# Optimization experiments

Measured on AMD Instinct MI355X. Metric: run time of the kernel, lower is better.

The kernel has to match this reference:

```python
import jax, jax.numpy as jnp
import numpy as np
import math

C = 512
GROUPS = 32
EPS = 1e-06


def group_norm(x, w, b):
    # x: [B, C, H, W]; 32 groups over channels
    B, Cc, H, W = x.shape
    xg = x.reshape(B, GROUPS, Cc // GROUPS, H, W)
    mu = jnp.mean(xg, axis=(2, 3, 4), keepdims=True)
    var = jnp.var(xg, axis=(2, 3, 4), keepdims=True)
    xn = ((xg - mu) * jax.lax.rsqrt(var + EPS)).reshape(B, Cc, H, W)
    return xn * w[None, :, None, None] + b[None, :, None, None]


def setup_inputs() -> dict:
    key = jax.random.key(0)
    ks = jax.random.split(key, 7)
    B, H, W = 2, 64, 64
    x = jax.random.normal(ks[0], (B, C, H, W), dtype=jnp.float32)
    gn_w = jnp.ones((C,), dtype=jnp.float32)
    gn_b = jnp.zeros((C,), dtype=jnp.float32)
    s = 1.0 / math.sqrt(C)
    qkv_w = jax.random.normal(ks[1], (3 * C, C), dtype=jnp.float32) * s
    qkv_b = jnp.zeros((3 * C,), dtype=jnp.float32)
    proj_w = jax.random.normal(ks[2], (C, C), dtype=jnp.float32) * s
    proj_b = jnp.zeros((C,), dtype=jnp.float32)
    return {"x": x, "gn_w": gn_w, "gn_b": gn_b, "qkv_w": qkv_w,
            "qkv_b": qkv_b, "proj_w": proj_w, "proj_b": proj_b}


def reference(x, gn_w, gn_b, qkv_w, qkv_b, proj_w, proj_b):
    residue = x
    B, Cc, H, W = x.shape
    N = H * W
    constant = 1.0 / math.sqrt(Cc)
    xn = group_norm(x, gn_w, gn_b)
    # 1x1 conv == channel matmul
    qkv = jnp.einsum('bchw,oc->bohw', xn, qkv_w) + qkv_b[None, :, None, None]
    q, k, v = jnp.split(qkv, 3, axis=1)
    q = q.reshape(B, Cc, N)
    k = k.reshape(B, Cc, N)
    v = v.reshape(B, Cc, N)
    # attn[b,i,j] = sum_c k[b,c,i] * q[b,c,j]   (k^T @ q, per original code)
    attn = jnp.einsum('bci,bcj->bij', k, q) * constant
    soft = jax.nn.softmax(attn, axis=2)  # softmax over q-index j, as in torch dim=2
    # output[b,c,i] = sum_j v[b,c,j] * soft[b,j,i]   (v @ soft)
    out = jnp.einsum('bcj,bji->bci', v, soft).reshape(B, Cc, H, W)
    proj = jnp.einsum('bchw,oc->bohw', out, proj_w) + proj_b[None, :, None, None]
    return residue + proj
```

## Files before the change

### kernel.cpp

```cpp
#include <hip/hip_runtime.h>
#include <hip/hip_bf16.h>
#include <math.h>

typedef unsigned short ushort_t;
typedef __attribute__((ext_vector_type(8))) unsigned short ushort8;
typedef __attribute__((ext_vector_type(8))) __bf16 bf16x8;
typedef __attribute__((ext_vector_type(4))) float f32x4;

__device__ inline ushort_t f2b(float f) {
  __hip_bfloat16 h = __float2bfloat16(f);
  return __builtin_bit_cast(ushort_t, h);
}
__device__ inline float b2f(ushort_t u) {
  __hip_bfloat16 h = __builtin_bit_cast(__hip_bfloat16, u);
  return __bfloat162float(h);
}

__device__ inline void gload16(const ushort_t* g, ushort_t* l) {
  __builtin_amdgcn_global_load_lds(
      (const __attribute__((address_space(1))) unsigned int*)g,
      (__attribute__((address_space(3))) unsigned int*)l, 16, 0, 0);
}

__device__ inline void xcd_swz(int& bx, int& by, int& bz) {
  const int nx = gridDim.x, ny = gridDim.y;
  const int nwg = nx * ny * gridDim.z;
  const int orig = blockIdx.x + nx * (blockIdx.y + ny * blockIdx.z);
  const int q = nwg >> 3, r = nwg & 7, xcd = orig & 7, loc = orig >> 3;
  const int wg = (xcd < r ? xcd * (q + 1) : r * (q + 1) + (xcd - r) * q) + loc;
  bx = wg % nx;
  by = (wg / nx) % ny;
  bz = wg / (nx * ny);
}

__global__ __launch_bounds__(256) void prep_stats(
    const float* __restrict__ qkv_w, const float* __restrict__ proj_w,
    const float* __restrict__ x, ushort_t* __restrict__ qkvw,
    ushort_t* __restrict__ projw, float* __restrict__ stats) {
  const int tid = threadIdx.x;
  if (blockIdx.x < 4096) {
    int idx = blockIdx.x * 256 + tid;
    const int NQ = 1536 * 512;
    if (idx < NQ) {
      qkvw[idx] = f2b(qkv_w[idx]);
    } else {
      int j = idx - NQ;
      if (j < 512 * 512) projw[j] = f2b(proj_w[j]);
    }
    return;
  }
  const int bg = blockIdx.x - 4096;
  const float4* xv = (const float4*)(x + (size_t)bg * 65536);
  float s = 0.f, ss = 0.f;
  for (int i = tid; i < 16384; i += 256) {
    float4 v = xv[i];
    s += v.x + v.y + v.z + v.w;
    ss += v.x * v.x + v.y * v.y + v.z * v.z + v.w * v.w;
  }
  __shared__ float red[8];
  for (int off = 32; off > 0; off >>= 1) {
    s += __shfl_down(s, off);
    ss += __shfl_down(ss, off);
  }
  if ((tid & 63) == 0) { red[tid >> 6] = s; red[4 + (tid >> 6)] = ss; }
  __syncthreads();
  if (tid == 0) {
    float st = red[0] + red[1] + red[2] + red[3];
    float sst = red[4] + red[5] + red[6] + red[7];
    float mean = st * (1.f / 65536.f);
    float var = sst * (1.f / 65536.f) - mean * mean;
    stats[bg * 2] = mean;
    stats[bg * 2 + 1] = rsqrtf(var + 1e-6f);
  }
}

__global__ __launch_bounds__(256) void gn_apply_t(
    const float* __restrict__ x, const float* __restrict__ w,
    const float* __restrict__ bgn, const float* __restrict__ stats,
    ushort_t* __restrict__ xnT) {
  __shared__ ushort_t tile[64][68];
  const int b = blockIdx.z;
  const int p0 = blockIdx.x * 64, c0 = blockIdx.y * 64;
  const int tid = threadIdx.x;
  const float* xb = x + ((size_t)b * 512 + c0) * 4096 + p0;
  const int tc = tid >> 4, tp = (tid & 15) * 4;
#pragma unroll
  for (int pass = 0; pass < 4; ++pass) {
    int c = pass * 16 + tc;
    int cg = c0 + c;
    float mean = stats[(b * 32 + (cg >> 4)) * 2];
    float inv = stats[(b * 32 + (cg >> 4)) * 2 + 1];
    float wc = w[cg] * inv;
    float bc = bgn[cg] - mean * wc;
    float4 v = *(const float4*)(xb + (size_t)c * 4096 + tp);
    tile[c][tp] = f2b(v.x * wc + bc);
    tile[c][tp + 1] = f2b(v.y * wc + bc);
    tile[c][tp + 2] = f2b(v.z * wc + bc);
    tile[c][tp + 3] = f2b(v.w * wc + bc);
  }
  __syncthreads();
  const int c8 = (tid & 7) * 8;
#pragma unroll
  for (int pass = 0; pass < 2; ++pass) {
    int p = pass * 32 + (tid >> 3);
    ushort8 u;
#pragma unroll
    for (int e = 0; e < 8; ++e) u[e] = tile[c8 + e][p];
    *(ushort8*)(xnT + ((size_t)b * 4096 + p0 + p) * 512 + c0 + c8) = u;
  }
}

__global__ __launch_bounds__(512, 2) void gemm8(
    const ushort_t* __restrict__ A, const ushort_t* __restrict__ B,
    ushort_t* __restrict__ Cg, float* __restrict__ smp, int N, int K, int lda,
    int ldb, size_t sA, size_t sB, size_t sC, float scale) {
  __shared__ __align__(16) ushort_t smem[66560];
  ushort_t* Asl = smem;
  ushort_t* Bsl = smem + 32768;
  float* s_sum = (float*)(smem + 65536);

  int bx, by, bz;
  xcd_swz(bx, by, bz);
  const ushort_t* Ab = A + bz * sA;
  const ushort_t* Bb = B + bz * sB;
  const int bm0 = by * 256, bn0 = bx * 256;
  const int tid = threadIdx.x;
  const int w = tid >> 6, lane = tid & 63;
  const int wr = w >> 2, wc = w & 3;
  const int fr = lane & 15, fq = lane >> 4;

  const int srow = tid >> 3, scb = tid & 7;
  const int ssw = scb ^ (srow & 7);
  const ushort_t* aS = Ab + (size_t)(bm0 + srow) * lda + ssw * 8;
  const ushort_t* bS = Bb + (size_t)(bn0 + srow) * ldb + ssw * 8;

  auto stage_a = [&](int s, int kk) {
#pragma unroll
    for (int g = 0; g < 4; ++g)
      gload16(aS + (size_t)(g * 64) * lda + kk,
              &Asl[s * 16384 + g * 4096 + w * 512]);
  };
  auto stage_b = [&](int s, int kk) {
#pragma unroll
    for (int g = 0; g < 4; ++g)
      gload16(bS + (size_t)(g * 64) * ldb + kk,
              &Bsl[s * 16384 + g * 4096 + w * 512]);
  };

  f32x4 acc[8][4] = {};
  bf16x8 a_r[4][2], b_r[4][2];

  auto read_a = [&](int s, int mh) {
#pragma unroll
    for (int mi = 0; mi < 4; ++mi) {
      int row = wr * 128 + mh * 64 + mi * 16 + fr;
#pragma unroll
      for (int ks = 0; ks < 2; ++ks) {
        int blk = ((ks * 4 + fq) ^ (row & 7)) * 8;
        a_r[mi][ks] = *(const bf16x8*)&Asl[s * 16384 + row * 64 + blk];
      }
    }
  };
  auto read_b = [&](int s, int nh) {
#pragma unroll
    for (int ni = 0; ni < 2; ++ni) {
      int row = wc * 64 + nh * 32 + ni * 16 + fr;
#pragma unroll
      for (int ks = 0; ks < 2; ++ks) {
        int blk = ((ks * 4 + fq) ^ (row & 7)) * 8;
        b_r[nh * 2 + ni][ks] = *(const bf16x8*)&Bsl[s * 16384 + row * 64 + blk];
      }
    }
  };
  auto phase_mfma = [&](int mh, int nh) {
    __builtin_amdgcn_s_setprio(1);
#pragma unroll
    for (int ks = 0; ks < 2; ++ks)
#pragma unroll
      for (int mi = 0; mi < 4; ++mi)
#pragma unroll
        for (int ni = 0; ni < 2; ++ni)
          acc[mh * 4 + mi][nh * 2 + ni] =
              __builtin_amdgcn_mfma_f32_16x16x32_bf16(
                  a_r[mi][ks], b_r[nh * 2 + ni][ks],
                  acc[mh * 4 + mi][nh * 2 + ni], 0, 0, 0);
    __builtin_amdgcn_s_setprio(0);
  };

  const int nt = K >> 6;
  stage_b(0, 0);
  stage_a(0, 0);
  if (nt > 1) {
    stage_b(1, 64);
    stage_a(1, 64);
    asm volatile("s_waitcnt vmcnt(8)" ::: "memory");
  } else {
    asm volatile("s_waitcnt vmcnt(0)" ::: "memory");
  }
  __builtin_amdgcn_s_barrier();

  for (int t = 0; t < nt; ++t) {
    const int s = t & 1;
    const int kk2 = (t + 2) << 6;
    const bool st2 = (t + 2) < nt;
    read_b(s, 0);
    read_b(s, 1);
    read_a(s, 0);
    phase_mfma(0, 0);
    phase_mfma(0, 1);
    read_a(s, 1);
    phase_mfma(1, 0);
    __builtin_amdgcn_s_barrier();
    if (st2) {
      stage_b(s, kk2);
      stage_a(s, kk2);
    }
    phase_mfma(1, 1);
    if (st2)
      asm volatile("s_waitcnt vmcnt(8)" ::: "memory");
    else if (t + 1 < nt)
      asm volatile("s_waitcnt vmcnt(0)" ::: "memory");
    __builtin_amdgcn_s_barrier();
  }
  __syncthreads();

  const size_t cbase = (size_t)bz * sC;
  float csum[4] = {0.f, 0.f, 0.f, 0.f};
  ushort_t* tp = smem;
#pragma unroll
  for (int step = 0; step < 2; ++step) {
    if (wr == step) {
#pragma unroll
      for (int mi = 0; mi < 8; ++mi)
#pragma unroll
        for (int ni = 0; ni < 4; ++ni)
#pragma unroll
          for (int r = 0; r < 4; ++r) {
            int lr = mi * 16 + fq * 4 + r;
            int col = wc * 64 + ni * 16 + fr;
            float e = __expf(fminf(acc[mi][ni][r] * scale, 76.f));
            csum[ni] += e;
            int cblk = col >> 3;
            tp[lr * 256 + (((cblk ^ (lr & 7)) << 3) | (col & 7))] = f2b(e);
          }
    }
    __syncthreads();
#pragma unroll
    for (int k = 0; k < 8; ++k) {
      int row = (tid >> 5) + 16 * k;
      int cblk = tid & 31;
      ushort8 u = *(const ushort8*)&tp[row * 256 + ((cblk ^ (row & 7)) << 3)];
      size_t off =
          cbase + (size_t)(bm0 + step * 128 + row) * N + bn0 + cblk * 8;
      __builtin_nontemporal_store(u, (ushort8*)(Cg + off));
    }
    __syncthreads();
  }
#pragma unroll
  for (int ni = 0; ni < 4; ++ni) {
    float s = csum[ni];
    s += __shfl_xor(s, 16);
    s += __shfl_xor(s, 32);
    if (lane < 16) s_sum[wr * 256 + wc * 64 + ni * 16 + lane] = s;
  }
  __syncthreads();
  if (tid < 256) {
    smp[((size_t)bz * 16 + by) * 4096 + bn0 + tid] =
        s_sum[tid] + s_sum[256 + tid];
  }
}

template <int EPI, int SPLIT>
__global__ __launch_bounds__(256, 2) void gemm_pl(
    const ushort_t* __restrict__ A, const ushort_t* __restrict__ B,
    void* __restrict__ Cg, const float* __restrict__ bias,
    const float* __restrict__ colsc, int N, int K, int lda, int ldb,
    size_t sA, size_t sB, size_t sC, size_t sSp) {
  __shared__ __align__(16) ushort_t Al[2][128 * 64];
  __shared__ __align__(16) ushort_t Bl[2][128 * 64];
  __shared__ float s_alpha[128];
  int bx, by, bzt;
  xcd_swz(bx, by, bzt);
  const int bz = bzt / SPLIT, sp = bzt % SPLIT;
  const ushort_t* Ab = A + bz * sA + (size_t)sp * K;
  const ushort_t* Bb = B + bz * sB + (size_t)sp * K;
  const int bm0 = by * 128, bn0 = bx * 128;
  const int tid = threadIdx.x;
  const int w = tid >> 6, lane = tid & 63;
  const int wm = (w >> 1) * 64, wn = (w & 1) * 64;
  const int fr = lane & 15, fq = lane >> 4;

  if constexpr (EPI == 3) {
    if (tid < 128) {
      float S = 0.f;
#pragma unroll
      for (int rc = 0; rc < 16; ++rc)
        S += colsc[((size_t)bz * 16 + rc) * 4096 + bn0 + tid];
      s_alpha[tid] = 1.f / S;
    }
    asm volatile("s_waitcnt lgkmcnt(0)" ::: "memory");
  }

  const int srow = tid >> 3, scb = tid & 7;
  const int ssw = scb ^ (srow & 7);
  const ushort_t* aS = Ab + (size_t)(bm0 + srow) * lda + ssw * 8;
  const ushort_t* bS = Bb + (size_t)(bn0 + srow) * ldb + ssw * 8;

  auto stage = [&](int s, int kk) {
#pragma unroll
    for (int g = 0; g < 4; ++g)
      gload16(aS + (size_t)(g * 32) * lda + kk, &Al[s][g * 2048 + w * 512]);
#pragma unroll
    for (int g = 0; g < 4; ++g)
      gload16(bS + (size_t)(g * 32) * ldb + kk, &Bl[s][g * 2048 + w * 512]);
  };

  f32x4 acc[4][4] = {};
  bf16x8 a_r[4][2], b_r[4][2];

  const int nt = K >> 6;
  stage(0, 0);
  if (nt > 1) {
    stage(1, 64);
    asm volatile("s_waitcnt vmcnt(8)" ::: "memory");
  } else {
    asm volatile("s_waitcnt vmcnt(0)" ::: "memory");
  }
  __builtin_amdgcn_s_barrier();

  for (int t = 0; t < nt; ++t) {
    const int s = t & 1;
#pragma unroll
    for (int mi = 0; mi < 4; ++mi) {
      int row = wm + mi * 16 + fr;
#pragma unroll
      for (int ks = 0; ks < 2; ++ks) {
        int blk = ((ks * 4 + fq) ^ (row & 7)) * 8;
        a_r[mi][ks] = *(const bf16x8*)&Al[s][row * 64 + blk];
      }
    }
#pragma unroll
    for (int ni = 0; ni < 4; ++ni) {
      int row = wn + ni * 16 + fr;
#pragma unroll
      for (int ks = 0; ks < 2; ++ks) {
        int blk = ((ks * 4 + fq) ^ (row & 7)) * 8;
        b_r[ni][ks] = *(const bf16x8*)&Bl[s][row * 64 + blk];
      }
    }
    __builtin_amdgcn_s_barrier();
    __builtin_amdgcn_s_setprio(1);
#pragma unroll
    for (int ks = 0; ks < 2; ++ks)
#pragma unroll
      for (int mi = 0; mi < 4; ++mi)
#pragma unroll
        for (int ni = 0; ni < 2; ++ni)
          acc[mi][ni] = __builtin_amdgcn_mfma_f32_16x16x32_bf16(
              a_r[mi][ks], b_r[ni][ks], acc[mi][ni], 0, 0, 0);
    __builtin_amdgcn_s_setprio(0);
    __builtin_amdgcn_s_barrier();
    if (t + 2 < nt) stage(s, (t + 2) << 6);
    __builtin_amdgcn_s_setprio(1);
#pragma unroll
    for (int ks = 0; ks < 2; ++ks)
#pragma unroll
      for (int mi = 0; mi < 4; ++mi)
#pragma unroll
        for (int ni = 2; ni < 4; ++ni)
          acc[mi][ni] = __builtin_amdgcn_mfma_f32_16x16x32_bf16(
              a_r[mi][ks], b_r[ni][ks], acc[mi][ni], 0, 0, 0);
    __builtin_amdgcn_s_setprio(0);
    if (t + 2 < nt)
      asm volatile("s_waitcnt vmcnt(8)" ::: "memory");
    else if (t + 1 < nt)
      asm volatile("s_waitcnt vmcnt(0)" ::: "memory");
    __builtin_amdgcn_s_barrier();
  }

  const int r0 = (lane >> 4) * 4;
  const size_t cbase = (size_t)sp * sSp + (size_t)bz * sC;
#pragma unroll
  for (int mi = 0; mi < 4; mi++) {
#pragma unroll
    for (int r = 0; r < 4; r++) {
      int gm = bm0 + wm + mi * 16 + r0 + r;
#pragma unroll
      for (int ni = 0; ni < 4; ni++) {
        int gn = bn0 + wn + ni * 16 + fr;
        float v = acc[mi][ni][r];
        size_t off = cbase + (size_t)gm * N + gn;
        if constexpr (EPI == 0) {
          ((ushort_t*)Cg)[off] = f2b(v + bias[gn]);
        } else if constexpr (EPI == 3) {
          ((ushort_t*)Cg)[off] = f2b(v * s_alpha[gn - bn0]);
        } else {
          __builtin_nontemporal_store(f2b(v), (ushort_t*)Cg + off);
        }
      }
    }
  }
}

__global__ __launch_bounds__(256) void finalize(
    const ushort_t* __restrict__ part, const float* __restrict__ x,
    const float* __restrict__ pb, float* __restrict__ out) {
  __shared__ float tile[64][68];
  const int b = blockIdx.z;
  const int p0 = blockIdx.x * 64, o0 = blockIdx.y * 64;
  const int tid = threadIdx.x;
  const int tp = tid >> 2, to = (tid & 3) * 16;
  const size_t base = ((size_t)b * 4096 + p0 + tp) * 512 + o0 + to;
  ushort8 u0 = *(const ushort8*)(part + base);
  ushort8 u1 = *(const ushort8*)(part + base + 8);
  ushort8 v0 = *(const ushort8*)(part + 4194304 + base);
  ushort8 v1 = *(const ushort8*)(part + 4194304 + base + 8);
#pragma unroll
  for (int e = 0; e < 8; ++e) {
    tile[tp][to + e] = b2f(u0[e]) + b2f(v0[e]);
    tile[tp][to + 8 + e] = b2f(u1[e]) + b2f(v1[e]);
  }
  __syncthreads();
  const int wo = tid >> 2, wp = (tid & 3) * 16;
  float bias = pb[o0 + wo];
  const float* xr = x + ((size_t)b * 512 + o0 + wo) * 4096 + p0 + wp;
  float* orow = out + ((size_t)b * 512 + o0 + wo) * 4096 + p0 + wp;
#pragma unroll
  for (int e = 0; e < 16; ++e)
    orow[e] = tile[wp + e][wo] + xr[e] + bias;
}

extern "C" void kernel_launch(void* const* d_in, const int* in_sizes, int n_in,
                              void* d_out, int out_size, void* d_ws,
                              size_t ws_size, hipStream_t stream) {
  const float* x = (const float*)d_in[0];
  const float* gn_w = (const float*)d_in[1];
  const float* gn_b = (const float*)d_in[2];
  const float* qkv_w = (const float*)d_in[3];
  const float* qkv_b = (const float*)d_in[4];
  const float* proj_w = (const float*)d_in[5];
  const float* proj_b = (const float*)d_in[6];
  float* out = (float*)d_out;

  char* ws = (char*)d_ws;
  ushort_t* xnT   = (ushort_t*)(ws);
  ushort_t* Wpp   = (ushort_t*)(ws);
  ushort_t* qkvw  = (ushort_t*)(ws + 8388608);
  ushort_t* projw = (ushort_t*)(ws + 9961472);
  float*    stats = (float*)(ws + 10485760);
  ushort_t* qkvT  = (ushort_t*)(ws + 10486272);
  ushort_t* part  = (ushort_t*)(ws + 10486272);
  ushort_t* P     = (ushort_t*)(ws + 35652096);
  float*    smp   = (float*)(ws + 102760960);

  const float scale = 0.04419417382415922f;
  const size_t sXN = 2097152, sQKV = (size_t)4096 * 1536, sP = 16777216;

  prep_stats<<<4160, 256, 0, stream>>>(qkv_w, proj_w, x, qkvw, projw, stats);
  gn_apply_t<<<dim3(64, 8, 2), 256, 0, stream>>>(x, gn_w, gn_b, stats, xnT);
  gemm_pl<0, 1><<<dim3(12, 64, 1), 256, 0, stream>>>(
      xnT, qkvw, qkvT, qkv_b, nullptr, 1536, 512, 512, 512, 0, 0, 0, 0);
  gemm8<<<dim3(16, 16, 2), 512, 0, stream>>>(
      qkvT, qkvT + 512, P, smp, 4096, 512, 1536, 1536, sQKV, sQKV, sP, scale);
  gemm_pl<3, 1><<<dim3(32, 4, 2), 256, 0, stream>>>(
      projw, qkvT + 1024, Wpp, nullptr, smp, 4096, 512, 512, 1536, 0, sQKV,
      sXN, 0);
  gemm_pl<5, 2><<<dim3(4, 32, 4), 256, 0, stream>>>(
      P, Wpp, part, nullptr, nullptr, 512, 2048, 4096, 4096, sP, sXN, sXN,
      4194304);
  finalize<<<dim3(64, 8, 2), 256, 0, stream>>>(part, x, proj_b, out);
}
```

Before: 172.3 us.

## Halve gemm K-tile to 32 to cut LDS and raise occupancy

Shrinks the GEMM K-step from 64 to 32, halving shared memory per block (about 66 KB down to 33 KB) and raising launch bounds to allow 4 blocks per CU. Staging, swizzle and fragment loads are rewritten for 32-wide rows, and the MFMA loop is restructured so all A/B fragments are read before a barrier, with the next-tile prefetch issued between the two MFMA halves. The aim is more resident waves to hide latency, at the cost of twice as many barriers and iterations and tighter register limits that may cause spills with the 8x4 accumulator array.

```diff
diff --git a/kernel.cpp b/kernel.cpp
--- a/kernel.cpp
+++ b/kernel.cpp
@@ -110,14 +110,12 @@
   }
 }
 
-__global__ __launch_bounds__(512, 2) void gemm8(
+__global__ __launch_bounds__(512, 4) void gemm8(
     const ushort_t* __restrict__ A, const ushort_t* __restrict__ B,
     ushort_t* __restrict__ Cg, float* __restrict__ smp, int N, int K, int lda,
     int ldb, size_t sA, size_t sB, size_t sC, float scale) {
-  __shared__ __align__(16) ushort_t smem[66560];
-  ushort_t* Asl = smem;
-  ushort_t* Bsl = smem + 32768;
-  float* s_sum = (float*)(smem + 65536);
+  __shared__ __align__(16) ushort_t smem[33792];
+  float* s_sum = (float*)(smem + 32768);
 
   int bx, by, bz;
   xcd_swz(bx, by, bz);
@@ -129,95 +127,66 @@
   const int wr = w >> 2, wc = w & 3;
   const int fr = lane & 15, fq = lane >> 4;
 
-  const int srow = tid >> 3, scb = tid & 7;
-  const int ssw = scb ^ (srow & 7);
+  const int srow = tid >> 2, scb = tid & 3;
+  const int ssw = scb ^ ((srow >> 1) & 3);
   const ushort_t* aS = Ab + (size_t)(bm0 + srow) * lda + ssw * 8;
   const ushort_t* bS = Bb + (size_t)(bn0 + srow) * ldb + ssw * 8;
 
-  auto stage_a = [&](int s, int kk) {
-#pragma unroll
-    for (int g = 0; g < 4; ++g)
-      gload16(aS + (size_t)(g * 64) * lda + kk,
-              &Asl[s * 16384 + g * 4096 + w * 512]);
+  auto stage = [&](int s, int kk) {
+#pragma unroll
+    for (int g = 0; g < 2; ++g)
+      gload16(aS + (size_t)(g * 128) * lda + kk,
+              &smem[s * 8192 + g * 4096 + w * 512]);
+#pragma unroll
+    for (int g = 0; g < 2; ++g)
+      gload16(bS + (size_t)(g * 128) * ldb + kk,
+              &smem[16384 + s * 8192 + g * 4096 + w * 512]);
   };
-  auto stage_b = [&](int s, int kk) {
-#pragma unroll
-    for (int g = 0; g < 4; ++g)
-      gload16(bS + (size_t)(g * 64) * ldb + kk,
-              &Bsl[s * 16384 + g * 4096 + w * 512]);
-  };
 
   f32x4 acc[8][4] = {};
-  bf16x8 a_r[4][2], b_r[4][2];
-
-  auto read_a = [&](int s, int mh) {
-#pragma unroll
-    for (int mi = 0; mi < 4; ++mi) {
-      int row = wr * 128 + mh * 64 + mi * 16 + fr;
-#pragma unroll
-      for (int ks = 0; ks < 2; ++ks) {
-        int blk = ((ks * 4 + fq) ^ (row & 7)) * 8;
-        a_r[mi][ks] = *(const bf16x8*)&Asl[s * 16384 + row * 64 + blk];
-      }
-    }
-  };
-  auto read_b = [&](int s, int nh) {
-#pragma unroll
-    for (int ni = 0; ni < 2; ++ni) {
-      int row = wc * 64 + nh * 32 + ni * 16 + fr;
-#pragma unroll
-      for (int ks = 0; ks < 2; ++ks) {
-        int blk = ((ks * 4 + fq) ^ (row & 7)) * 8;
-        b_r[nh * 2 + ni][ks] = *(const bf16x8*)&Bsl[s * 16384 + row * 64 + blk];
-      }
-    }
-  };
-  auto phase_mfma = [&](int mh, int nh) {
-    __builtin_amdgcn_s_setprio(1);
-#pragma unroll
-    for (int ks = 0; ks < 2; ++ks)
-#pragma unroll
-      for (int mi = 0; mi < 4; ++mi)
-#pragma unroll
-        for (int ni = 0; ni < 2; ++ni)
-          acc[mh * 4 + mi][nh * 2 + ni] =
-              __builtin_amdgcn_mfma_f32_16x16x32_bf16(
-                  a_r[mi][ks], b_r[nh * 2 + ni][ks],
-                  acc[mh * 4 + mi][nh * 2 + ni], 0, 0, 0);
-    __builtin_amdgcn_s_setprio(0);
-  };
-
-  const int nt = K >> 6;
-  stage_b(0, 0);
-  stage_a(0, 0);
-  if (nt > 1) {
-    stage_b(1, 64);
-    stage_a(1, 64);
-    asm volatile("s_waitcnt vmcnt(8)" ::: "memory");
-  } else {
-    asm volatile("s_waitcnt vmcnt(0)" ::: "memory");
-  }
+  bf16x8 a_r[8], b_r[4];
+
+  const int nt = K >> 5;
+  stage(0, 0);
+  stage(1, 32);
+  asm volatile("s_waitcnt vmcnt(4)" ::: "memory");
   __builtin_amdgcn_s_barrier();
 
   for (int t = 0; t < nt; ++t) {
     const int s = t & 1;
-    const int kk2 = (t + 2) << 6;
-    const bool st2 = (t + 2) < nt;
-    read_b(s, 0);
-    read_b(s, 1);
-    read_a(s, 0);
-    phase_mfma(0, 0);
-    phase_mfma(0, 1);
-    read_a(s, 1);
-    phase_mfma(1, 0);
-    __builtin_amdgcn_s_barrier();
-    if (st2) {
-      stage_b(s, kk2);
-      stage_a(s, kk2);
-    }
-    phase_mfma(1, 1);
-    if (st2)
-      asm volatile("s_waitcnt vmcnt(8)" ::: "memory");
+#pragma unroll
+    for (int mi = 0; mi < 8; ++mi) {
+      int row = wr * 128 + mi * 16 + fr;
+      int blk = fq ^ ((row >> 1) & 3);
+      a_r[mi] = *(const bf16x8*)&smem[s * 8192 + row * 32 + blk * 8];
+    }
+#pragma unroll
+    for (int ni = 0; ni < 4; ++ni) {
+      int row = wc * 64 + ni * 16 + fr;
+      int blk = fq ^ ((row >> 1) & 3);
+      b_r[ni] = *(const bf16x8*)&smem[16384 + s * 8192 + row * 32 + blk * 8];
+    }
+    __builtin_amdgcn_s_barrier();
+    __builtin_amdgcn_s_setprio(1);
+#pragma unroll
+    for (int mi = 0; mi < 8; ++mi)
+#pragma unroll
+      for (int ni = 0; ni < 2; ++ni)
+        acc[mi][ni] = __builtin_amdgcn_mfma_f32_16x16x32_bf16(
+            a_r[mi], b_r[ni], acc[mi][ni], 0, 0, 0);
+    __builtin_amdgcn_s_setprio(0);
+    __builtin_amdgcn_s_barrier();
+    if (t + 2 < nt) stage(s, (t + 2) << 5);
+    __builtin_amdgcn_s_setprio(1);
+#pragma unroll
+    for (int mi = 0; mi < 8; ++mi)
+#pragma unroll
+      for (int ni = 2; ni < 4; ++ni)
+        acc[mi][ni] = __builtin_amdgcn_mfma_f32_16x16x32_bf16(
+            a_r[mi], b_r[ni], acc[mi][ni], 0, 0, 0);
+    __builtin_amdgcn_s_setprio(0);
+    if (t + 2 < nt)
+      asm volatile("s_waitcnt vmcnt(4)" ::: "memory");
     else if (t + 1 < nt)
       asm volatile("s_waitcnt vmcnt(0)" ::: "memory");
     __builtin_amdgcn_s_barrier();
```

Result: slower. 495.9 us (+187.8%).
